# Performance work log

Hardware: AMD Instinct MI355X
Metric: run time of the kernel (lower is better)

## Reference

```python
import jax, jax.numpy as jnp
import numpy as np

B, H, I = 4096, 128, 128


def setup_inputs() -> dict:
    key = jax.random.key(0)
    ks = jax.random.split(key, 9)
    # xavier_uniform for W1/W2: fan_in = 2H*2I, fan_out = H*2I (torch treats dim0 as fan_out for >2D differently,
    # but we only need a plausible init; exact init values don't affect correctness of the math)
    def xavier(k, shape):
        fan_in = shape[1] * shape[2] if len(shape) == 3 else shape[0]
        fan_out = shape[0] * shape[2] if len(shape) == 3 else shape[1]
        lim = np.sqrt(6.0 / (fan_in + fan_out))
        return jax.random.uniform(k, shape, jnp.float32, -lim, lim)
    W1 = xavier(ks[0], (H, 2 * H, 2 * I))
    W2 = xavier(ks[1], (H, 2 * H, 2 * I))
    W3 = xavier(ks[2], (2 * H, H))
    fan_in, fan_out = 2 * H * 2 * I, H * 2 * I
    lim = float(np.sqrt(3.0 / (0.5 * (fan_in + fan_out))))
    b1 = jax.random.uniform(ks[3], (H,), jnp.float32, -lim, lim)
    b2 = jax.random.uniform(ks[4], (H,), jnp.float32, -lim, lim)
    in0 = jax.random.normal(ks[5], (B, I), jnp.float32)
    in1 = jax.random.normal(ks[6], (B, I), jnp.float32)
    st0 = jax.random.normal(ks[7], (B, H), jnp.float32)
    st1 = jax.random.normal(ks[8], (B, H), jnp.float32)
    return {"in0": in0, "in1": in1, "st0": st0, "st1": st1,
            "W1": W1, "b1": b1, "W2": W2, "b2": b2, "W3": W3}


def reference(in0, in1, st0, st1, W1, b1, W2, b2, W3):
    s = jnp.concatenate([st0, st1], axis=1)  # [B, 2H]
    x = jnp.concatenate([in0, in1], axis=1)  # [B, 2I]
    # Trilinear contraction; same math as outer-product-then-contract:
    # einsum('ij,ik->ijk') then ('ijk,ljk->il')  ==  'bj,bk,ljk->bl'
    m1 = jnp.einsum('bj,bk,ljk->bl', s, x, W1)  # [B, H]
    m2 = jnp.einsum('bj,bk,ljk->bl', s, x, W2)  # [B, H]
    u = jax.nn.sigmoid(m2 + b2)
    state_tilda = jnp.tanh(m1 + b1)
    new_state = u * state_tilda + (1.0 - u) * (s @ W3)
    return new_state
```

## Files before the change

kernel.cpp:

```cpp
#include <hip/hip_runtime.h>
#include <hip/hip_bf16.h>
#include <stdint.h>


typedef short bf8 __attribute__((ext_vector_type(8)));
typedef float f32x4 __attribute__((ext_vector_type(4)));

static constexpr size_t WT_OFF  = 0;
static constexpr size_t XBF_OFF = 33554432 + 2097152;
static constexpr size_t MP_OFF  = XBF_OFF + 2097152;

__device__ __forceinline__ unsigned f2bf(float f) {
    unsigned u = __builtin_bit_cast(unsigned, f);
    return (u + 0x7fffu + ((u >> 16) & 1u)) >> 16;
}
__device__ __forceinline__ unsigned pack2bf(float a, float b) {
    return f2bf(a) | (f2bf(b) << 16);
}

__global__ void prep_wx(const float* __restrict__ W1, const float* __restrict__ W2,
                        const float* __restrict__ in0, const float* __restrict__ in1,
                        uint4* __restrict__ Wt, unsigned* __restrict__ x_bf) {
    int bx = blockIdx.x;
    if (bx < 8192) {
        const int tid  = threadIdx.x;
        const int lane = tid & 63, wave = tid >> 6;
        const unsigned f = bx * 4 + wave;
        const unsigned n16 = f >> 11;
        const unsigned kchunk = (f >> 1) & 1023u;
        const unsigned kst = f & 1u;
        const unsigned n = n16 * 16 + (lane & 15);
        const unsigned K = kchunk * 64 + kst * 32 + (lane >> 4) * 8;
        const float* src = (n < 128 ? W1 + ((size_t)n << 16)
                                    : W2 + ((size_t)(n - 128) << 16)) + K;
        float4 a = ((const float4*)src)[0];
        float4 b = ((const float4*)src)[1];
        uint4 o;
        o.x = pack2bf(a.x, a.y); o.y = pack2bf(a.z, a.w);
        o.z = pack2bf(b.x, b.y); o.w = pack2bf(b.z, b.w);
        Wt[(size_t)f * 64 + lane] = o;
    } else {
        unsigned v = (bx - 8192) * 256 + threadIdx.x;
        unsigned b = v >> 6;
        unsigned j4 = (v & 63u) * 4u;
        const float* src = (j4 < 128) ? (in0 + (size_t)b * 128 + j4)
                                      : (in1 + (size_t)b * 128 + (j4 - 128));
        float4 a = *(const float4*)src;
        uint2 o;
        o.x = pack2bf(a.x, a.y);
        o.y = pack2bf(a.z, a.w);
        ((uint2*)x_bf)[v] = o;
    }
}

__launch_bounds__(256, 2)
__global__ void gemm_p(const unsigned char* __restrict__ Wt,
                       const float* __restrict__ st0, const float* __restrict__ st1,
                       const __hip_bfloat16* __restrict__ x_bf,
                       float* __restrict__ Mpart) {
    const int bx = blockIdx.x;
    const int ks = bx & 7;
    const int nt = (bx >> 3) & 1;
    const int mt = bx >> 4;
    const int b0 = mt << 7, n0 = nt << 7;
    const int tid  = threadIdx.x;
    const int lane = tid & 63, wave = tid >> 6;
    const int l15 = lane & 15, l4 = lane >> 4;

    __shared__ __align__(16) float Sl[32 * 132];
    for (int idx = tid; idx < 4096; idx += 256) {
        int r = idx >> 5, j = idx & 31;
        int jg = ks * 32 + j;
        float v = (jg < 128) ? st0[(size_t)(b0 + r) * 128 + jg]
                             : st1[(size_t)(b0 + r) * 128 + (jg - 128)];
        Sl[j * 132 + r] = v;
    }
    __syncthreads();

    const int n16_0 = __builtin_amdgcn_readfirstlane(nt * 8 + wave * 2 + 0);
    const int n16_1 = __builtin_amdgcn_readfirstlane(nt * 8 + wave * 2 + 1);
    const unsigned char* wb0 = Wt + ((size_t)n16_0 << 21);
    const unsigned char* wb1 = Wt + ((size_t)n16_1 << 21);

    f32x4 racc[8][2];
    #pragma unroll
    for (int mf = 0; mf < 8; ++mf)
        #pragma unroll
        for (int nf = 0; nf < 2; ++nf)
            racc[mf][nf] = (f32x4){0.f, 0.f, 0.f, 0.f};
    const f32x4 zacc = (f32x4){0.f, 0.f, 0.f, 0.f};

    bf8 a[8][2];
    bf8 buf[2][2][2];

    unsigned vo = (unsigned)lane * 16u + (unsigned)ks * 262144u;

    for (int q = 0; q < 4; ++q) {
        #pragma unroll
        for (int mf = 0; mf < 8; ++mf) {
            const __hip_bfloat16* xp =
                x_bf + (size_t)((b0 + mf * 16 + l15) * 256 + q * 64 + l4 * 8);
            a[mf][0] = *(const bf8*)(xp);
            a[mf][1] = *(const bf8*)(xp + 32);
        }
        buf[0][0][0] = *(const bf8*)(wb0 + vo);
        buf[0][0][1] = *(const bf8*)(wb0 + vo + 1024);
        buf[0][1][0] = *(const bf8*)(wb1 + vo);
        buf[0][1][1] = *(const bf8*)(wb1 + vo + 1024);
        vo += 8192;

        const float* svp = Sl + l4 * 4;

        for (int jb = 0; jb < 4; ++jb) {
            #pragma unroll
            for (int jj = 0; jj < 8; ++jj) {
                const int pp = jj & 1;
                buf[pp ^ 1][0][0] = *(const bf8*)(wb0 + vo);
                buf[pp ^ 1][0][1] = *(const bf8*)(wb0 + vo + 1024);
                buf[pp ^ 1][1][0] = *(const bf8*)(wb1 + vo);
                buf[pp ^ 1][1][1] = *(const bf8*)(wb1 + vo + 1024);
                vo += 8192;
                f32x4 sv[8];
                #pragma unroll
                for (int mf = 0; mf < 8; ++mf)
                    sv[mf] = *(const f32x4*)(svp + mf * 16);
                svp += 132;
                {
                    f32x4 mA, mB;
#define PAIR_(MF, NF, MD) \
    MD = __builtin_amdgcn_mfma_f32_16x16x32_bf16(a[MF][0], buf[pp][NF][0], zacc, 0, 0, 0); \
    MD = __builtin_amdgcn_mfma_f32_16x16x32_bf16(a[MF][1], buf[pp][NF][1], MD, 0, 0, 0);
#define ACC_(MF, NF, MS) racc[MF][NF] += sv[MF] * MS;
                    PAIR_(0, 0, mA)
                    PAIR_(1, 0, mB)  ACC_(0, 0, mA)
                    PAIR_(2, 0, mA)  ACC_(1, 0, mB)
                    PAIR_(3, 0, mB)  ACC_(2, 0, mA)
                    PAIR_(4, 0, mA)  ACC_(3, 0, mB)
                    PAIR_(5, 0, mB)  ACC_(4, 0, mA)
                    PAIR_(6, 0, mA)  ACC_(5, 0, mB)
                    PAIR_(7, 0, mB)  ACC_(6, 0, mA)
                    PAIR_(0, 1, mA)  ACC_(7, 0, mB)
                    PAIR_(1, 1, mB)  ACC_(0, 1, mA)
                    PAIR_(2, 1, mA)  ACC_(1, 1, mB)
                    PAIR_(3, 1, mB)  ACC_(2, 1, mA)
                    PAIR_(4, 1, mA)  ACC_(3, 1, mB)
                    PAIR_(5, 1, mB)  ACC_(4, 1, mA)
                    PAIR_(6, 1, mA)  ACC_(5, 1, mB)
                    PAIR_(7, 1, mB)  ACC_(6, 1, mA)
                                     ACC_(7, 1, mB)
#undef PAIR_
#undef ACC_
                }
            }
        }
        vo += 2048 - 33 * 8192;
    }

    float* mp = Mpart + ((size_t)ks << 20);
    #pragma unroll
    for (int mf = 0; mf < 8; ++mf)
        #pragma unroll
        for (int nf = 0; nf < 2; ++nf) {
            int b = b0 + mf * 16 + l4 * 4;
            int n = n0 + wave * 32 + nf * 16 + l15;
            #pragma unroll
            for (int r = 0; r < 4; ++r)
                mp[(size_t)(b + r) * 256 + n] = racc[mf][nf][r];
        }
}

__global__ void epilogue(const float* __restrict__ st0, const float* __restrict__ st1,
                         const float* __restrict__ b1, const float* __restrict__ b2,
                         const float* __restrict__ W3, const float* __restrict__ Mpart,
                         float* __restrict__ out) {
    const int tid = threadIdx.x;
    const int h = tid & 127, rg = tid >> 7;
    const int bbase = blockIdx.x * 4;
    __shared__ float srow[4][256];
    #pragma unroll
    for (int i = 0; i < 4; ++i) {
        int idx = i * 256 + tid;
        int r = idx >> 8, j = idx & 255;
        float v = (j < 128) ? st0[(size_t)(bbase + r) * 128 + j]
                            : st1[(size_t)(bbase + r) * 128 + (j - 128)];
        srow[r][j] = v;
    }
    __syncthreads();
    float acc0 = 0.f, acc1 = 0.f;
    #pragma unroll 8
    for (int j = 0; j < 256; ++j) {
        float w = W3[j * 128 + h];
        acc0 += srow[rg][j] * w;
        acc1 += srow[rg + 2][j] * w;
    }
    float accs[2] = {acc0, acc1};
    float bb1 = b1[h], bb2 = b2[h];
    #pragma unroll
    for (int i = 0; i < 2; ++i) {
        int b = bbase + rg + i * 2;
        float m1 = 0.f, m2 = 0.f;
        #pragma unroll
        for (int k = 0; k < 8; ++k) {
            m1 += Mpart[((size_t)k << 20) + (size_t)b * 256 + h];
            m2 += Mpart[((size_t)k << 20) + (size_t)b * 256 + 128 + h];
        }
        float u = 1.0f / (1.0f + expf(-(m2 + bb2)));
        float t = tanhf(m1 + bb1);
        out[(size_t)b * 128 + h] = u * t + (1.0f - u) * accs[i];
    }
}

extern "C" void kernel_launch(void* const* d_in, const int* in_sizes, int n_in,
                              void* d_out, int out_size, void* d_ws, size_t ws_size,
                              hipStream_t stream) {
    const float* in0 = (const float*)d_in[0];
    const float* in1 = (const float*)d_in[1];
    const float* st0 = (const float*)d_in[2];
    const float* st1 = (const float*)d_in[3];
    const float* W1  = (const float*)d_in[4];
    const float* b1  = (const float*)d_in[5];
    const float* W2  = (const float*)d_in[6];
    const float* b2  = (const float*)d_in[7];
    const float* W3  = (const float*)d_in[8];
    float* out = (float*)d_out;
    char* ws = (char*)d_ws;

    unsigned char* Wt   = (unsigned char*)(ws + WT_OFF);
    unsigned*      x_bf = (unsigned*)(ws + XBF_OFF);
    float*         Mp   = (float*)(ws + MP_OFF);

    prep_wx<<<9216, 256, 0, stream>>>(W1, W2, in0, in1, (uint4*)Wt, x_bf);
    gemm_p<<<512, 256, 0, stream>>>(Wt, st0, st1, (const __hip_bfloat16*)x_bf, Mp);
    epilogue<<<1024, 256, 0, stream>>>(st0, st1, b1, b2, W3, Mp, out);
}
```

Before: 258.8 us.

## Stage weight bf16 conversion through swizzled LDS and raise MFMA wave priority

```diff
diff --git a/kernel.cpp b/kernel.cpp
--- a/kernel.cpp
+++ b/kernel.cpp
@@ -22,25 +22,40 @@
                         const float* __restrict__ in0, const float* __restrict__ in1,
                         uint4* __restrict__ Wt, unsigned* __restrict__ x_bf) {
     int bx = blockIdx.x;
-    if (bx < 8192) {
-        const int tid  = threadIdx.x;
-        const int lane = tid & 63, wave = tid >> 6;
-        const unsigned f = bx * 4 + wave;
-        const unsigned n16 = f >> 11;
-        const unsigned kchunk = (f >> 1) & 1023u;
-        const unsigned kst = f & 1u;
-        const unsigned n = n16 * 16 + (lane & 15);
-        const unsigned K = kchunk * 64 + kst * 32 + (lane >> 4) * 8;
-        const float* src = (n < 128 ? W1 + ((size_t)n << 16)
-                                    : W2 + ((size_t)(n - 128) << 16)) + K;
-        float4 a = ((const float4*)src)[0];
-        float4 b = ((const float4*)src)[1];
-        uint4 o;
-        o.x = pack2bf(a.x, a.y); o.y = pack2bf(a.z, a.w);
-        o.z = pack2bf(b.x, b.y); o.w = pack2bf(b.z, b.w);
-        Wt[(size_t)f * 64 + lane] = o;
+    if (bx < 2048) {
+        const int tid = threadIdx.x;
+        const int n16 = bx >> 7;
+        const int g   = bx & 127;
+        __shared__ __align__(16) unsigned short lds[16 * 512];
+        const float* base = (n16 < 8)
+            ? (W1 + ((size_t)(n16 * 16) << 16))
+            : (W2 + ((size_t)((n16 - 8) * 16) << 16));
+        #pragma unroll
+        for (int t = 0; t < 8; ++t) {
+            int idx = t * 256 + tid;
+            int r  = idx >> 7;
+            int c4 = idx & 127;
+            float4 v = *(const float4*)(base + ((size_t)r << 16) + g * 512 + c4 * 4);
+            uint2 o;
+            o.x = pack2bf(v.x, v.y);
+            o.y = pack2bf(v.z, v.w);
+            unsigned byte = (unsigned)(r * 1024 + c4 * 8) ^ (unsigned)((r & 7) << 4);
+            *(uint2*)((char*)lds + byte) = o;
+        }
+        __syncthreads();
+        uint4* outp = Wt + (size_t)(n16 * 1024 + g * 8) * 2 * 64;
+        #pragma unroll
+        for (int t = 0; t < 4; ++t) {
+            int idx  = t * 256 + tid;
+            int fl   = idx >> 6;
+            int lane = idx & 63;
+            int r = lane & 15;
+            int k = (fl >> 1) * 64 + (fl & 1) * 32 + (lane >> 4) * 8;
+            unsigned byte = (unsigned)(r * 1024 + k * 2) ^ (unsigned)((r & 7) << 4);
+            outp[fl * 64 + lane] = *(const uint4*)((const char*)lds + byte);
+        }
     } else {
-        unsigned v = (bx - 8192) * 256 + threadIdx.x;
+        unsigned v = (bx - 2048) * 256 + threadIdx.x;
         unsigned b = v >> 6;
         unsigned j4 = (v & 63u) * 4u;
         const float* src = (j4 < 128) ? (in0 + (size_t)b * 128 + j4)
@@ -125,6 +140,7 @@
                 for (int mf = 0; mf < 8; ++mf)
                     sv[mf] = *(const f32x4*)(svp + mf * 16);
                 svp += 132;
+                __builtin_amdgcn_s_setprio(1);
                 {
                     f32x4 mA, mB;
 #define PAIR_(MF, NF, MD) \
@@ -151,6 +167,7 @@
 #undef PAIR_
 #undef ACC_
                 }
+                __builtin_amdgcn_s_setprio(0);
             }
         }
         vo += 2048 - 33 * 8192;
@@ -229,7 +246,7 @@
     unsigned*      x_bf = (unsigned*)(ws + XBF_OFF);
     float*         Mp   = (float*)(ws + MP_OFF);
 
-    prep_wx<<<9216, 256, 0, stream>>>(W1, W2, in0, in1, (uint4*)Wt, x_bf);
+    prep_wx<<<3072, 256, 0, stream>>>(W1, W2, in0, in1, (uint4*)Wt, x_bf);
     gemm_p<<<512, 256, 0, stream>>>(Wt, st0, st1, (const __hip_bfloat16*)x_bf, Mp);
     epilogue<<<1024, 256, 0, stream>>>(st0, st1, b1, b2, W3, Mp, out);
 }
```

Measured after the change: 256.6 us. No clear change (-0.8%).
